# Kernel optimization log

Measured on AMD Instinct MI355X. Metric: run time of the kernel, lower is better.

Reference implementation:

```python
import jax, jax.numpy as jnp
import numpy as np

S, B, F, U = 8, 65536, 256, 256  # N_species, N_batch, N_feats, N_units (depth=2)


def setup_inputs() -> dict:
    key = jax.random.key(0)
    ks = jax.random.split(key, 9)
    b = jax.random.normal(ks[0], (S, B, F), dtype=jnp.float32)
    # Per-species weights stacked along species axis (equivalent to ModuleList of Linears).
    # nn.Linear default init: U(-1/sqrt(fan_in), 1/sqrt(fan_in)) -- exact dist doesn't matter
    # for a correctness baseline; scale similarly.
    def lin(k, fan_in, shape):
        lim = 1.0 / np.sqrt(fan_in)
        return jax.random.uniform(k, shape, dtype=jnp.float32, minval=-lim, maxval=lim)
    W1 = lin(ks[1], F, (S, F, U)); b1 = lin(ks[2], F, (S, U))
    W2 = lin(ks[3], U, (S, U, U)); b2 = lin(ks[4], U, (S, U))
    W3 = lin(ks[5], U, (S, U, U)); b3 = lin(ks[6], U, (S, U))
    W4 = lin(ks[7], U, (S, U, 1)); b4 = lin(ks[8], U, (S, 1))
    return {"b": b, "W1": W1, "b1": b1, "W2": W2, "b2": b2,
            "W3": W3, "b3": b3, "W4": W4, "b4": b4}


def _leaky(x):
    return jnp.where(x >= 0, x, 0.1 * x)  # LeakyReLU(0.1)


def reference(b, W1, b1, W2, b2, W3, b3, W4, b4):
    # depth == 2 path. Dropout(p=0.01) is identity in eval mode.
    # Per-species batched GEMMs: (S,B,in) x (S,in,out) -> (S,B,out)
    x = _leaky(jnp.einsum('sbf,sfu->sbu', b, W1) + b1[:, None, :])
    x = _leaky(jnp.einsum('sbu,suv->sbv', x, W2) + b2[:, None, :])
    x = _leaky(jnp.einsum('sbu,suv->sbv', x, W3) + b3[:, None, :])
    A = jnp.einsum('sbu,suo->sbo', x, W4) + b4[:, None, :]  # (S, B, 1)
    return jax.nn.sigmoid(A.sum(axis=0))  # (B, 1)
```

## Files before the change

kernel.cpp:

```cpp
#include <hip/hip_runtime.h>

typedef __bf16 bf16x8 __attribute__((ext_vector_type(8)));
typedef float  f32x4  __attribute__((ext_vector_type(4)));
typedef float  fvec4  __attribute__((ext_vector_type(4)));

#define NSPEC 8
#define NB    65536
#define NF    256

__global__ __launch_bounds__(256) void wconv_kernel(
    const float* __restrict__ W1, const float* __restrict__ W2,
    const float* __restrict__ W3, __bf16* __restrict__ WT)
{
    __shared__ float tile[32][33];
    int bid = blockIdx.x;
    int l   = bid >> 9;
    int rem = bid & 511;
    int s   = rem >> 6;
    int tt  = rem & 63;
    int ti  = tt >> 3, tj = tt & 7;
    const float* W   = (l == 0) ? W1 : (l == 1) ? W2 : W3;
    const float* ibs = W + (size_t)s * 65536;
    int c  = threadIdx.x & 31;
    int r0 = threadIdx.x >> 5;
#pragma unroll
    for (int k = 0; k < 4; ++k) {
        int r = r0 + k * 8;
        tile[r][c] = ibs[(ti * 32 + r) * 256 + tj * 32 + c];
    }
    __syncthreads();
    __bf16* obs = WT + ((size_t)(l * 8 + s)) * 65536;
#pragma unroll
    for (int k = 0; k < 4; ++k) {
        int r = r0 + k * 8;
        obs[(tj * 32 + r) * 256 + ti * 32 + c] = (__bf16)tile[c][r];
    }
}

#define GLLD(gp, lp)                                                     \
    __builtin_amdgcn_global_load_lds(                                    \
        (const __attribute__((address_space(1))) char*)(gp),             \
        (__attribute__((address_space(3))) char*)(lp), 16, 0, 0)

#define BAR()                                                            \
    do {                                                                 \
        __builtin_amdgcn_sched_barrier(0);                               \
        asm volatile("s_waitcnt lgkmcnt(0)" ::: "memory");               \
        __builtin_amdgcn_s_barrier();                                    \
        __builtin_amdgcn_sched_barrier(0);                               \
    } while (0)

__global__ __launch_bounds__(256, 2) void mlp_kernel(
    const float* __restrict__ bIn, const float* __restrict__ b1,
    const float* __restrict__ b2,  const float* __restrict__ b3,
    const float* __restrict__ W4,  const float* __restrict__ b4,
    const __bf16* __restrict__ WT, float* __restrict__ P)
{
    __shared__ __align__(16) __bf16 act[64 * 256];
    __shared__ __align__(16) char  wlds[3][16384];

    const int t    = threadIdx.x;
    const int lane = t & 63;
    const int wave = t >> 6;
    const int l15  = lane & 15;
    const int g    = lane >> 4;
    const int wv   = wave * 64;
    const int s    = blockIdx.x >> 10;
    const int row0 = (blockIdx.x & 1023) * 64;
    const int swzB = l15 << 4;
    char* const pA = (char*)act;

    int gll_off[4];
#pragma unroll
    for (int i = 0; i < 4; ++i) {
        int v = wv + i * 16 + (lane >> 2);
        int q = (lane & 3) ^ ((v >> 1) & 3);
        gll_off[i] = v * 512 + q * 16;
    }

    const char* const wt0 = (const char*)(WT + ((size_t)(0 * 8 + s) << 16));
    const char* const wt1 = (const char*)(WT + ((size_t)(1 * 8 + s) << 16));
    const char* const wt2 = (const char*)(WT + ((size_t)(2 * 8 + s) << 16));

#define ISSUE_CHUNK(wtb, gci)                                            \
    do {                                                                 \
        char* lp0 = (char*)&wlds[(gci) % 3][wave * 4096];                \
        GLLD((wtb) + gll_off[0] + ((gci) & 7) * 64, lp0);                \
        GLLD((wtb) + gll_off[1] + ((gci) & 7) * 64, lp0 + 1024);         \
        GLLD((wtb) + gll_off[2] + ((gci) & 7) * 64, lp0 + 2048);         \
        GLLD((wtb) + gll_off[3] + ((gci) & 7) * 64, lp0 + 3072);         \
    } while (0)

#define READ_SET(AF, BF, gci, kslice)                                    \
    do {                                                                 \
        const char* wbuf_ = (const char*)wlds[(gci) % 3];                \
        _Pragma("unroll")                                                \
        for (int m_ = 0; m_ < 4; ++m_) {                                 \
            int row_ = wv + m_ * 16 + l15;                               \
            AF[m_] = *(const bf16x8*)(wbuf_ + row_ * 64 +                \
                                      ((g ^ ((row_ >> 1) & 3)) << 4));   \
        }                                                                \
        _Pragma("unroll")                                                \
        for (int n_ = 0; n_ < 4; ++n_)                                   \
            BF[n_] = *(const bf16x8*)(pA + (n_ * 16 + l15) * 512 +       \
                                      (((kslice) * 64 + g * 16) ^ swzB));\
    } while (0)

#define MFMA_SET(AF, BF)                                                 \
    do {                                                                 \
        __builtin_amdgcn_s_setprio(1);                                   \
        _Pragma("unroll")                                                \
        for (int m_ = 0; m_ < 4; ++m_)                                   \
            _Pragma("unroll")                                            \
            for (int n_ = 0; n_ < 4; ++n_)                               \
                acc[m_][n_] = __builtin_amdgcn_mfma_f32_16x16x32_bf16(   \
                    AF[m_], BF[n_], acc[m_][n_], 0, 0, 0);               \
        __builtin_amdgcn_s_setprio(0);                                   \
    } while (0)

    fvec4 bias[3][4];
#pragma unroll
    for (int l = 0; l < 3; ++l) {
        const float* bl = (l == 0 ? b1 : l == 1 ? b2 : b3) + s * 256;
#pragma unroll
        for (int m = 0; m < 4; ++m)
            bias[l][m] = *(const fvec4*)(bl + wv + m * 16 + g * 4);
    }

    const float* src = bIn + ((size_t)s * NB + row0) * NF;
#pragma unroll
    for (int it = 0; it < 16; ++it) {
        int flat = it * 1024 + t * 4;
        int r = flat >> 8;
        int f = flat & 255;
        fvec4 v = __builtin_nontemporal_load((const fvec4*)(src + flat));
        union { __bf16 h[4]; unsigned long long q; } pk;
        pk.h[0] = (__bf16)v[0]; pk.h[1] = (__bf16)v[1];
        pk.h[2] = (__bf16)v[2]; pk.h[3] = (__bf16)v[3];
        *(unsigned long long*)(pA + r * 512 + ((f * 2) ^ ((r & 15) << 4))) = pk.q;
    }

    ISSUE_CHUNK(wt0, 0);
    ISSUE_CHUNK(wt0, 1);
    ISSUE_CHUNK(wt0, 2);
    BAR();

#pragma unroll
    for (int l = 0; l < 3; ++l) {
        const int c0 = l * 8;
        f32x4 acc[4][4];
#pragma unroll
        for (int m = 0; m < 4; ++m)
#pragma unroll
            for (int n = 0; n < 4; ++n)
                acc[m][n] = (f32x4){0.f, 0.f, 0.f, 0.f};

        bf16x8 afA[4], bfrA[4], afB[4], bfrB[4];
        asm volatile("s_waitcnt vmcnt(8)" ::: "memory");
        READ_SET(afA, bfrA, c0, 0);

#pragma unroll
        for (int ks = 0; ks < 8; ++ks) {
            const int c = c0 + ks;
            if (ks < 7) {
                if (c <= 21) asm volatile("s_waitcnt vmcnt(4)" ::: "memory");
                else         asm volatile("s_waitcnt vmcnt(0)" ::: "memory");
                if ((ks & 1) == 0) READ_SET(afB, bfrB, c + 1, ks + 1);
                else               READ_SET(afA, bfrA, c + 1, ks + 1);
            }
            if ((ks & 1) == 0) MFMA_SET(afA, bfrA);
            else               MFMA_SET(afB, bfrB);
            asm volatile("s_waitcnt lgkmcnt(0)" ::: "memory");
            if (c + 3 <= 23) {
                const char* wtc = (c + 3 < 8) ? wt0 : (c + 3 < 16) ? wt1 : wt2;
                ISSUE_CHUNK(wtc, c + 3);
            }
            __builtin_amdgcn_sched_barrier(0);
        }

        BAR();

#pragma unroll
        for (int m = 0; m < 4; ++m) {
            int vbyte = (wv + m * 16 + g * 4) * 2;
#pragma unroll
            for (int n = 0; n < 4; ++n) {
                union { __bf16 h[4]; unsigned long long q; } pk;
#pragma unroll
                for (int j = 0; j < 4; ++j) {
                    float x = acc[m][n][j] + bias[l][m][j];
                    x = (x >= 0.f) ? x : 0.1f * x;
                    pk.h[j] = (__bf16)x;
                }
                *(unsigned long long*)(pA + (n * 16 + l15) * 512 + (vbyte ^ swzB)) = pk.q;
            }
        }
        BAR();
    }

    const int r4   = t >> 2;
    const int u0   = (t & 3) * 64;
    const int swz4 = (r4 & 15) << 4;
    const float* w4s = W4 + s * 256 + u0;
    float part = 0.f;
#pragma unroll
    for (int i = 0; i < 8; ++i) {
        bf16x8 x = *(const bf16x8*)(pA + r4 * 512 + (((u0 + i * 8) * 2) ^ swz4));
        fvec4 wlo = *(const fvec4*)(w4s + i * 8);
        fvec4 whi = *(const fvec4*)(w4s + i * 8 + 4);
        part += (float)x[0] * wlo[0] + (float)x[1] * wlo[1] +
                (float)x[2] * wlo[2] + (float)x[3] * wlo[3] +
                (float)x[4] * whi[0] + (float)x[5] * whi[1] +
                (float)x[6] * whi[2] + (float)x[7] * whi[3];
    }
    part += __shfl_xor(part, 1);
    part += __shfl_xor(part, 2);
    if ((t & 3) == 0) P[(size_t)s * NB + row0 + r4] = part + b4[s];
}

__global__ __launch_bounds__(256) void reduce_kernel(
    const float* __restrict__ P, float* __restrict__ out)
{
    int i = blockIdx.x * 256 + threadIdx.x;
    float a = 0.f;
#pragma unroll
    for (int sp = 0; sp < NSPEC; ++sp) a += P[(size_t)sp * NB + i];
    out[i] = 1.f / (1.f + __expf(-a));
}

extern "C" void kernel_launch(void* const* d_in, const int* in_sizes, int n_in,
                              void* d_out, int out_size, void* d_ws, size_t ws_size,
                              hipStream_t stream)
{
    const float* bIn = (const float*)d_in[0];
    const float* W1  = (const float*)d_in[1];
    const float* b1  = (const float*)d_in[2];
    const float* W2  = (const float*)d_in[3];
    const float* b2  = (const float*)d_in[4];
    const float* W3  = (const float*)d_in[5];
    const float* b3  = (const float*)d_in[6];
    const float* W4  = (const float*)d_in[7];
    const float* b4  = (const float*)d_in[8];
    __bf16* WT = (__bf16*)d_ws;
    float*  P  = (float*)((char*)d_ws + (3u << 20));

    wconv_kernel<<<1536, 256, 0, stream>>>(W1, W2, W3, WT);
    mlp_kernel<<<8192, 256, 0, stream>>>(bIn, b1, b2, b3, W4, b4, WT, P);
    reduce_kernel<<<NB / 256, 256, 0, stream>>>(P, (float*)d_out);
}
```

Measured before the change: 352.1 us.

## Load weight fragments directly into registers instead of staging through LDS

Weight chunks are no longer copied into a triple-buffered LDS ring with global_load_lds. Each wave now loads its A fragments straight from global memory into a three-deep register ring, relying on the compiler for wait counts. Biases move from registers into a small LDS array that is read during the epilogue. This frees about 48KB of LDS and removes the LDS write/read round trip for weights. The cost is higher register pressure, less control over load latency than the hand-placed vmcnt waits gave, and possibly stalls if the global loads do not finish in time.

Result: slower. 450.4 us (+27.9%).

```diff
diff --git a/kernel.cpp b/kernel.cpp
--- a/kernel.cpp
+++ b/kernel.cpp
@@ -37,11 +37,6 @@
     }
 }
 
-#define GLLD(gp, lp)                                                     \
-    __builtin_amdgcn_global_load_lds(                                    \
-        (const __attribute__((address_space(1))) char*)(gp),             \
-        (__attribute__((address_space(3))) char*)(lp), 16, 0, 0)
-
 #define BAR()                                                            \
     do {                                                                 \
         __builtin_amdgcn_sched_barrier(0);                               \
@@ -57,7 +52,7 @@
     const __bf16* __restrict__ WT, float* __restrict__ P)
 {
     __shared__ __align__(16) __bf16 act[64 * 256];
-    __shared__ __align__(16) char  wlds[3][16384];
+    __shared__ __align__(16) float  bias_lds[3][256];
 
     const int t    = threadIdx.x;
     const int lane = t & 63;
@@ -70,36 +65,21 @@
     const int swzB = l15 << 4;
     char* const pA = (char*)act;
 
-    int gll_off[4];
-#pragma unroll
-    for (int i = 0; i < 4; ++i) {
-        int v = wv + i * 16 + (lane >> 2);
-        int q = (lane & 3) ^ ((v >> 1) & 3);
-        gll_off[i] = v * 512 + q * 16;
-    }
-
     const char* const wt0 = (const char*)(WT + ((size_t)(0 * 8 + s) << 16));
     const char* const wt1 = (const char*)(WT + ((size_t)(1 * 8 + s) << 16));
     const char* const wt2 = (const char*)(WT + ((size_t)(2 * 8 + s) << 16));
 
-#define ISSUE_CHUNK(wtb, gci)                                            \
-    do {                                                                 \
-        char* lp0 = (char*)&wlds[(gci) % 3][wave * 4096];                \
-        GLLD((wtb) + gll_off[0] + ((gci) & 7) * 64, lp0);                \
-        GLLD((wtb) + gll_off[1] + ((gci) & 7) * 64, lp0 + 1024);         \
-        GLLD((wtb) + gll_off[2] + ((gci) & 7) * 64, lp0 + 2048);         \
-        GLLD((wtb) + gll_off[3] + ((gci) & 7) * 64, lp0 + 3072);         \
-    } while (0)
-
-#define READ_SET(AF, BF, gci, kslice)                                    \
-    do {                                                                 \
-        const char* wbuf_ = (const char*)wlds[(gci) % 3];                \
+#define WLOAD(DST, c)                                                    \
+    do {                                                                 \
+        const char* wb_ = ((c) < 8) ? wt0 : ((c) < 16) ? wt1 : wt2;      \
         _Pragma("unroll")                                                \
-        for (int m_ = 0; m_ < 4; ++m_) {                                 \
-            int row_ = wv + m_ * 16 + l15;                               \
-            AF[m_] = *(const bf16x8*)(wbuf_ + row_ * 64 +                \
-                                      ((g ^ ((row_ >> 1) & 3)) << 4));   \
-        }                                                                \
+        for (int m_ = 0; m_ < 4; ++m_)                                   \
+            DST[m_] = *(const bf16x8*)(wb_ + (wv + m_ * 16 + l15) * 512  \
+                                       + ((c) & 7) * 64 + g * 16);       \
+    } while (0)
+
+#define READ_B(BF, kslice)                                               \
+    do {                                                                 \
         _Pragma("unroll")                                                \
         for (int n_ = 0; n_ < 4; ++n_)                                   \
             BF[n_] = *(const bf16x8*)(pA + (n_ * 16 + l15) * 512 +       \
@@ -118,13 +98,11 @@
         __builtin_amdgcn_s_setprio(0);                                   \
     } while (0)
 
-    fvec4 bias[3][4];
-#pragma unroll
-    for (int l = 0; l < 3; ++l) {
-        const float* bl = (l == 0 ? b1 : l == 1 ? b2 : b3) + s * 256;
-#pragma unroll
-        for (int m = 0; m < 4; ++m)
-            bias[l][m] = *(const fvec4*)(bl + wv + m * 16 + g * 4);
+    if (t < 192) {
+        int bl  = t >> 6;
+        int off = (t & 63) * 4;
+        const float* bp = (bl == 0 ? b1 : bl == 1 ? b2 : b3) + s * 256 + off;
+        *(fvec4*)&bias_lds[bl][off] = *(const fvec4*)bp;
     }
 
     const float* src = bIn + ((size_t)s * NB + row0) * NF;
@@ -139,15 +117,16 @@
         pk.h[2] = (__bf16)v[2]; pk.h[3] = (__bf16)v[3];
         *(unsigned long long*)(pA + r * 512 + ((f * 2) ^ ((r & 15) << 4))) = pk.q;
     }
-
-    ISSUE_CHUNK(wt0, 0);
-    ISSUE_CHUNK(wt0, 1);
-    ISSUE_CHUNK(wt0, 2);
+    __builtin_amdgcn_sched_barrier(0);
+
+    bf16x8 wreg[3][4];
+    WLOAD(wreg[0], 0);
+    WLOAD(wreg[1], 1);
+    WLOAD(wreg[2], 2);
     BAR();
 
 #pragma unroll
     for (int l = 0; l < 3; ++l) {
-        const int c0 = l * 8;
         f32x4 acc[4][4];
 #pragma unroll
         for (int m = 0; m < 4; ++m)
@@ -155,26 +134,19 @@
             for (int n = 0; n < 4; ++n)
                 acc[m][n] = (f32x4){0.f, 0.f, 0.f, 0.f};
 
-        bf16x8 afA[4], bfrA[4], afB[4], bfrB[4];
-        asm volatile("s_waitcnt vmcnt(8)" ::: "memory");
-        READ_SET(afA, bfrA, c0, 0);
+        bf16x8 bfX[4], bfY[4];
+        READ_B(bfX, 0);
 
 #pragma unroll
         for (int ks = 0; ks < 8; ++ks) {
-            const int c = c0 + ks;
+            const int c = l * 8 + ks;
             if (ks < 7) {
-                if (c <= 21) asm volatile("s_waitcnt vmcnt(4)" ::: "memory");
-                else         asm volatile("s_waitcnt vmcnt(0)" ::: "memory");
-                if ((ks & 1) == 0) READ_SET(afB, bfrB, c + 1, ks + 1);
-                else               READ_SET(afA, bfrA, c + 1, ks + 1);
+                if ((ks & 1) == 0) READ_B(bfY, ks + 1);
+                else               READ_B(bfX, ks + 1);
             }
-            if ((ks & 1) == 0) MFMA_SET(afA, bfrA);
-            else               MFMA_SET(afB, bfrB);
-            asm volatile("s_waitcnt lgkmcnt(0)" ::: "memory");
-            if (c + 3 <= 23) {
-                const char* wtc = (c + 3 < 8) ? wt0 : (c + 3 < 16) ? wt1 : wt2;
-                ISSUE_CHUNK(wtc, c + 3);
-            }
+            if ((ks & 1) == 0) MFMA_SET(wreg[c % 3], bfX);
+            else               MFMA_SET(wreg[c % 3], bfY);
+            if (c + 3 <= 23) WLOAD(wreg[(c + 3) % 3], c + 3);
             __builtin_amdgcn_sched_barrier(0);
         }
 
@@ -182,13 +154,14 @@
 
 #pragma unroll
         for (int m = 0; m < 4; ++m) {
+            fvec4 bq = *(const fvec4*)&bias_lds[l][wv + m * 16 + g * 4];
             int vbyte = (wv + m * 16 + g * 4) * 2;
 #pragma unroll
             for (int n = 0; n < 4; ++n) {
                 union { __bf16 h[4]; unsigned long long q; } pk;
 #pragma unroll
                 for (int j = 0; j < 4; ++j) {
-                    float x = acc[m][n][j] + bias[l][m][j];
+                    float x = acc[m][n][j] + bq[j];
                     x = (x >= 0.f) ? x : 0.1f * x;
                     pk.h[j] = (__bf16)x;
                 }
```
